# Kernel optimization log

Measured on AMD Instinct MI355X. Metric: run time of the kernel, lower is better.

## Reference

```python
import jax, jax.numpy as jnp
from jax import lax
import numpy as np

B, P, S, K = 16, 4096, 1024, 16   # clouds, points/cloud, fps samples/cloud (ratio 0.25), knn k
IN_F, OUT_F = 256, 512
EPS = 1e-5


def setup_inputs() -> dict:
    key = jax.random.key(0)
    k1, k2, k3 = jax.random.split(key, 3)
    features = jax.random.normal(k1, (B * P, IN_F), jnp.float32)
    positions = jax.random.normal(k2, (B * P, 3), jnp.float32)
    batch = jnp.repeat(jnp.arange(B, dtype=jnp.int32), P)
    W = jax.random.normal(k3, (IN_F, OUT_F), jnp.float32) / np.sqrt(IN_F)
    b = jnp.zeros((OUT_F,), jnp.float32)
    gamma = jnp.ones((OUT_F,), jnp.float32)
    beta = jnp.zeros((OUT_F,), jnp.float32)
    return {"features": features, "positions": positions, "batch": batch,
            "W": W, "b": b, "gamma": gamma, "beta": beta}


def _fps_local(pos):
    """Farthest point sampling on one cloud. pos: [P,3] -> [S] int32 local indices.
    Deterministic start at index 0 (torch_cluster fps with random_start disabled)."""
    def step(carry, _):
        min_d, last = carry
        d = jnp.sum((pos - pos[last]) ** 2, axis=-1)
        min_d = jnp.minimum(min_d, d)
        nxt = jnp.argmax(min_d).astype(jnp.int32)
        return (min_d, nxt), last
    init = (jnp.full((pos.shape[0],), jnp.inf, pos.dtype), jnp.int32(0))
    _, idx = lax.scan(step, init, None, length=S)
    return idx


def _knn_local(q, x):
    """K nearest neighbors of queries q [S,F] among x [P,F] (squared L2). -> [S,K] int32."""
    d = jnp.sum(q * q, -1, keepdims=True) - 2.0 * (q @ x.T) + jnp.sum(x * x, -1)
    _, idx = lax.top_k(-d, K)
    return idx


def reference(features, positions, batch, W, b, gamma, beta):
    pos_b = positions.reshape(B, P, 3)
    feat_b = features.reshape(B, P, IN_F)

    # --- FPS on positions, per cloud ---
    fps_loc = jax.vmap(_fps_local)(pos_b)                      # [B,S]
    offsets = (jnp.arange(B, dtype=jnp.int32) * P)[:, None]    # [B,1]
    fps_glob = (fps_loc + offsets).reshape(-1)                 # [B*S]

    # --- MLP: Linear -> BatchNorm1d (training batch stats, biased var) -> ReLU ---
    h = features @ W + b                                       # [N,OUT_F]
    mu = jnp.mean(h, axis=0)
    var = jnp.var(h, axis=0)
    h = jax.nn.relu(gamma * (h - mu) * lax.rsqrt(var + EPS) + beta)

    # --- brute-force KNN in feature space: queries = features[fps_indices] ---
    q = jnp.take_along_axis(feat_b, fps_loc[..., None], axis=1)   # [B,S,IN_F]
    nn_loc = jax.vmap(_knn_local)(q, feat_b)                      # [B,S,K]
    nn_glob = nn_loc + offsets[..., None]                         # [B,S,K]

    # --- scatter max-pool: each query has exactly K neighbors -> max over K ---
    nb = h[nn_glob.reshape(-1)].reshape(B, S, K, OUT_F)
    new_features = jnp.max(nb, axis=2).reshape(B * S, OUT_F)

    return new_features, positions[fps_glob], batch[fps_glob]
```

## Files before the change

kernel.cpp:

```cpp
#include <hip/hip_runtime.h>
#include <cstddef>


#define TD_B   16
#define TD_P   4096
#define TD_S   1024
#define TD_K   16
#define TD_INF 256
#define TD_OUTF 512

typedef __attribute__((ext_vector_type(8))) _Float16 half8;
typedef __attribute__((ext_vector_type(4))) float    f32x4;

__device__ __forceinline__ unsigned short f2bf(float x) {
    unsigned u = __float_as_uint(x);
    unsigned r = (u + 0x7fffu + ((u >> 16) & 1u)) >> 16;
    return (unsigned short)r;
}

struct FpsSm {
    float4 p4[TD_P];
    int    sel[TD_S];
    unsigned long long kw[2][8];
};
struct GemmSm {
    float As[16 * 260];
    float Bs[16 * 128];
};
union SmU {
    FpsSm f; GemmSm g;
    char pad_[84000];
};

#define TD_DPPSTEP(k, ctl, bc)                                                          \
    {                                                                                   \
        unsigned yh_ = (unsigned)__builtin_amdgcn_update_dpp(                           \
            0, (int)(unsigned)((k) >> 32), (ctl), 0xf, 0xf, (bc));                      \
        unsigned yl_ = (unsigned)__builtin_amdgcn_update_dpp(                           \
            0, (int)(unsigned)(k), (ctl), 0xf, 0xf, (bc));                              \
        unsigned long long y_ = ((unsigned long long)yh_ << 32) | yl_;                  \
        if (y_ > (k)) (k) = y_;                                                         \
    }

__global__ __launch_bounds__(512)
void td_fused(const float* __restrict__ feat, const float* __restrict__ pos,
              const float* __restrict__ W, const float* __restrict__ bias,
              unsigned short* __restrict__ H, float* __restrict__ XX,
              int* __restrict__ FPSI, float* __restrict__ outP,
              float* __restrict__ outB) {
    __shared__ SmU sm;
    const int bx = blockIdx.x;
    const int t  = threadIdx.x;

    if (bx < 16) {
        __builtin_amdgcn_s_setprio(2);
        const int b = bx;
        const int w = t >> 6;
        float px[8], py[8], pz[8], md[8];
        int ni[8];
#pragma unroll
        for (int j = 0; j < 8; ++j) {
            int p = j * 512 + t;
            const float* pp = pos + (size_t)(b * TD_P + p) * 3;
            float x = pp[0], y = pp[1], z = pp[2];
            px[j] = x; py[j] = y; pz[j] = z;
            sm.f.p4[p] = make_float4(x, y, z, 0.0f);
            md[j] = __builtin_inff();
            ni[j] = ~p;
        }
        if (t == 0) sm.f.sel[0] = 0;
        __syncthreads();
        float lx = sm.f.p4[0].x, ly = sm.f.p4[0].y, lz = sm.f.p4[0].z;
        for (int s = 0; s < TD_S - 1; ++s) {
            double k[8];
#pragma unroll
            for (int j = 0; j < 8; ++j) {
                float dx = __fsub_rn(px[j], lx);
                float dy = __fsub_rn(py[j], ly);
                float dz = __fsub_rn(pz[j], lz);
                float d  = __fadd_rn(__fadd_rn(__fmul_rn(dx, dx), __fmul_rn(dy, dy)),
                                     __fmul_rn(dz, dz));
                float m  = fminf(md[j], d);
                md[j] = m;
                k[j] = __hiloint2double(__float_as_int(m), ni[j]);
            }
            double k01 = fmax(k[0], k[1]), k23 = fmax(k[2], k[3]);
            double k45 = fmax(k[4], k[5]), k67 = fmax(k[6], k[7]);
            double kk  = fmax(fmax(k01, k23), fmax(k45, k67));
            unsigned long long tk = (unsigned long long)__double_as_longlong(kk);
            TD_DPPSTEP(tk, 0x111, true)
            TD_DPPSTEP(tk, 0x112, true)
            TD_DPPSTEP(tk, 0x114, true)
            TD_DPPSTEP(tk, 0x118, true)
            TD_DPPSTEP(tk, 0x142, false)
            TD_DPPSTEP(tk, 0x143, false)
            const int par = s & 1;
            if ((t & 63) == 63) sm.f.kw[par][w] = tk;
            __syncthreads();
            const unsigned long long* kwp = sm.f.kw[par];
            double g01 = fmax(__longlong_as_double((long long)kwp[0]),
                              __longlong_as_double((long long)kwp[1]));
            double g23 = fmax(__longlong_as_double((long long)kwp[2]),
                              __longlong_as_double((long long)kwp[3]));
            double g45 = fmax(__longlong_as_double((long long)kwp[4]),
                              __longlong_as_double((long long)kwp[5]));
            double g67 = fmax(__longlong_as_double((long long)kwp[6]),
                              __longlong_as_double((long long)kwp[7]));
            double gk  = fmax(fmax(g01, g23), fmax(g45, g67));
            unsigned idx = ~(unsigned)__double2loint(gk);
            if (t == 0) sm.f.sel[s + 1] = (int)idx;
            float4 wp = sm.f.p4[idx];
            lx = wp.x; ly = wp.y; lz = wp.z;
        }
        __syncthreads();
        for (int s = t; s < TD_S; s += 512) {
            int li = sm.f.sel[s];
            int og = b * TD_S + s;
            float4 wp = sm.f.p4[li];
            outP[og * 3 + 0] = wp.x;
            outP[og * 3 + 1] = wp.y;
            outP[og * 3 + 2] = wp.z;
            outB[og] = (float)b;
            FPSI[og] = b * TD_P + li;
        }
    } else if (bx < 16 + 1024) {
        const int gb = bx - 16;
        const int mb = gb >> 2, nb = gb & 3;
        const int tm = t >> 4, tn = t & 15;
        float acc[8][8];
#pragma unroll
        for (int i = 0; i < 8; ++i)
#pragma unroll
            for (int j = 0; j < 8; ++j) acc[i][j] = 0.0f;
        float* As = sm.g.As;
        float* Bs = sm.g.Bs;
        for (int kc = 0; kc < 16; ++kc) {
#pragma unroll
            for (int p2 = 0; p2 < 2; ++p2) {
                int f4 = t + 512 * p2;
                int r = f4 >> 2, c4 = f4 & 3;
                float4 v = *(const float4*)&feat[(size_t)(mb * 256 + r) * 256 + kc * 16 + c4 * 4];
                As[(c4 * 4 + 0) * 260 + r] = v.x;
                As[(c4 * 4 + 1) * 260 + r] = v.y;
                As[(c4 * 4 + 2) * 260 + r] = v.z;
                As[(c4 * 4 + 3) * 260 + r] = v.w;
            }
            {
                int kk = t >> 5, n4 = t & 31;
                float4 v = *(const float4*)&W[(size_t)(kc * 16 + kk) * 512 + nb * 128 + n4 * 4];
                *(float4*)&Bs[kk * 128 + n4 * 4] = v;
            }
            __syncthreads();
#pragma unroll
            for (int kk = 0; kk < 16; ++kk) {
                float4 a0 = *(float4*)&As[kk * 260 + tm * 8];
                float4 a1 = *(float4*)&As[kk * 260 + tm * 8 + 4];
                float4 b0 = *(float4*)&Bs[kk * 128 + tn * 8];
                float4 b1 = *(float4*)&Bs[kk * 128 + tn * 8 + 4];
                float av[8] = {a0.x, a0.y, a0.z, a0.w, a1.x, a1.y, a1.z, a1.w};
                float bv2[8] = {b0.x, b0.y, b0.z, b0.w, b1.x, b1.y, b1.z, b1.w};
#pragma unroll
                for (int i = 0; i < 8; ++i)
#pragma unroll
                    for (int j = 0; j < 8; ++j)
                        acc[i][j] = fmaf(av[i], bv2[j], acc[i][j]);
            }
            __syncthreads();
        }
        float4 bb0 = *(const float4*)&bias[nb * 128 + tn * 8];
        float4 bb1 = *(const float4*)&bias[nb * 128 + tn * 8 + 4];
        float bsv[8] = {bb0.x, bb0.y, bb0.z, bb0.w, bb1.x, bb1.y, bb1.z, bb1.w};
#pragma unroll
        for (int i = 0; i < 8; ++i) {
            int row = mb * 256 + tm * 8 + i;
            uint4 pk;
            pk.x = (unsigned)f2bf(acc[i][0] + bsv[0]) | ((unsigned)f2bf(acc[i][1] + bsv[1]) << 16);
            pk.y = (unsigned)f2bf(acc[i][2] + bsv[2]) | ((unsigned)f2bf(acc[i][3] + bsv[3]) << 16);
            pk.z = (unsigned)f2bf(acc[i][4] + bsv[4]) | ((unsigned)f2bf(acc[i][5] + bsv[5]) << 16);
            pk.w = (unsigned)f2bf(acc[i][6] + bsv[6]) | ((unsigned)f2bf(acc[i][7] + bsv[7]) << 16);
            *(uint4*)&H[(size_t)row * 512 + nb * 128 + tn * 8] = pk;
        }
    } else {
        const int xb = bx - 1040;
        const int w = t >> 6, lane = t & 63;
#pragma unroll
        for (int it = 0; it < 8; ++it) {
            int r = xb * 64 + w * 8 + it;
            float4 v = *(const float4*)&feat[(size_t)r * 256 + lane * 4];
            float s = v.x * v.x + v.y * v.y + v.z * v.z + v.w * v.w;
#pragma unroll
            for (int off = 32; off > 0; off >>= 1) s += __shfl_down(s, off, 64);
            if (lane == 0) XX[r] = s;
        }
    }
}

__global__ __launch_bounds__(256)
void td_stats(const unsigned short* __restrict__ H, float* __restrict__ P1,
              float* __restrict__ P2) {
    const int rb = blockIdx.x, t = threadIdx.x;
    float s1a = 0, s2a = 0, s1b = 0, s2b = 0;
    for (int r = 0; r < 256; ++r) {
        const unsigned* hp = (const unsigned*)(H + (size_t)(rb * 256 + r) * 512);
        unsigned u = hp[t];
        float lo = __uint_as_float(u << 16);
        float hi = __uint_as_float(u & 0xffff0000u);
        s1a += lo; s2a = fmaf(lo, lo, s2a);
        s1b += hi; s2b = fmaf(hi, hi, s2b);
    }
    P1[rb * 512 + 2 * t] = s1a; P1[rb * 512 + 2 * t + 1] = s1b;
    P2[rb * 512 + 2 * t] = s2a; P2[rb * 512 + 2 * t + 1] = s2b;
}

__global__ __launch_bounds__(512)
void td_bnfin(const float* __restrict__ P1, const float* __restrict__ P2,
              const float* __restrict__ gamma, const float* __restrict__ beta,
              float* __restrict__ SS) {
    const int ch = threadIdx.x;
    float s1 = 0, s2 = 0;
    for (int rb = 0; rb < 256; ++rb) { s1 += P1[rb * 512 + ch]; s2 += P2[rb * 512 + ch]; }
    const float invN = 1.0f / 65536.0f;
    float mu  = s1 * invN;
    float var = s2 * invN - mu * mu;
    float sc  = gamma[ch] * (1.0f / sqrtf(var + 1e-5f));
    float sh  = beta[ch] - mu * sc;
    SS[ch] = sc; SS[512 + ch] = sh;
}

__global__ __launch_bounds__(256, 2)
void td_knn2(const float* __restrict__ feat, const float* __restrict__ XX,
             const int* __restrict__ FPSI, float* __restrict__ PD,
             int* __restrict__ PI) {
    __shared__ union {
        _Float16 x[2][32][264];
        float    dt[128][33];
    } sm;
    __shared__ float QQs[128];
    __shared__ int   QR[128];

    const int bx = blockIdx.x, t = threadIdx.x;
    const int b = bx & 15, r2 = bx >> 4;
    const int qq8 = r2 >> 2, seg = r2 & 3;
    const int cb = b * TD_P;
    const int segbase = cb + seg * 1024;

    if (t < 128) {
        int gr = FPSI[b * TD_S + qq8 * 128 + t];
        QR[t] = gr; QQs[t] = XX[gr];
    }
    __syncthreads();

    const int w = t >> 6, lane = t & 63;
    const int m = lane & 15, quad = lane >> 4;

    half8 qh[2][8], ql[2][8];
#pragma unroll
    for (int qs = 0; qs < 2; ++qs) {
        const float* qp = feat + (size_t)QR[w * 32 + qs * 16 + m] * 256;
#pragma unroll
        for (int ks = 0; ks < 8; ++ks) {
            float4 f0 = *(const float4*)(qp + ks * 32 + quad * 8);
            float4 f1 = *(const float4*)(qp + ks * 32 + quad * 8 + 4);
            float fv[8] = {f0.x, f0.y, f0.z, f0.w, f1.x, f1.y, f1.z, f1.w};
            half8 h, l;
#pragma unroll
            for (int j = 0; j < 8; ++j) {
                _Float16 hv = (_Float16)fv[j];
                h[j] = hv;
                l[j] = (_Float16)(fv[j] - (float)hv);
            }
            qh[qs][ks] = h; ql[qs][ks] = l;
        }
    }

    float sd[16]; int si[16];
#pragma unroll
    for (int r = 0; r < 16; ++r) { sd[r] = __builtin_inff(); si[r] = 0x7fffffff; }

    const int xrow = t >> 3, part = t & 7;

    for (int ct = 0; ct < 32; ++ct) {
        __syncthreads();
        {
            const float* xp = feat + (size_t)(segbase + ct * 32 + xrow) * 256 + part * 32;
#pragma unroll
            for (int s2 = 0; s2 < 4; ++s2) {
                float4 f0 = *(const float4*)(xp + s2 * 8);
                float4 f1 = *(const float4*)(xp + s2 * 8 + 4);
                float fv[8] = {f0.x, f0.y, f0.z, f0.w, f1.x, f1.y, f1.z, f1.w};
                half8 h, l;
#pragma unroll
                for (int j = 0; j < 8; ++j) {
                    _Float16 hv = (_Float16)fv[j];
                    h[j] = hv;
                    l[j] = (_Float16)(fv[j] - (float)hv);
                }
                *(half8*)&sm.x[0][xrow][part * 32 + s2 * 8] = h;
                *(half8*)&sm.x[1][xrow][part * 32 + s2 * 8] = l;
            }
        }
        __syncthreads();
        f32x4 acc[2][2];
#pragma unroll
        for (int qs = 0; qs < 2; ++qs) { acc[qs][0] = (f32x4)0.0f; acc[qs][1] = (f32x4)0.0f; }
#pragma unroll
        for (int ks = 0; ks < 8; ++ks) {
            half8 xh0 = *(half8*)&sm.x[0][m][ks * 32 + quad * 8];
            half8 xl0 = *(half8*)&sm.x[1][m][ks * 32 + quad * 8];
            half8 xh1 = *(half8*)&sm.x[0][16 + m][ks * 32 + quad * 8];
            half8 xl1 = *(half8*)&sm.x[1][16 + m][ks * 32 + quad * 8];
#pragma unroll
            for (int qs = 0; qs < 2; ++qs) {
                acc[qs][0] = __builtin_amdgcn_mfma_f32_16x16x32_f16(ql[qs][ks], xh0, acc[qs][0], 0, 0, 0);
                acc[qs][0] = __builtin_amdgcn_mfma_f32_16x16x32_f16(qh[qs][ks], xl0, acc[qs][0], 0, 0, 0);
                acc[qs][0] = __builtin_amdgcn_mfma_f32_16x16x32_f16(qh[qs][ks], xh0, acc[qs][0], 0, 0, 0);
                acc[qs][1] = __builtin_amdgcn_mfma_f32_16x16x32_f16(ql[qs][ks], xh1, acc[qs][1], 0, 0, 0);
                acc[qs][1] = __builtin_amdgcn_mfma_f32_16x16x32_f16(qh[qs][ks], xl1, acc[qs][1], 0, 0, 0);
                acc[qs][1] = __builtin_amdgcn_mfma_f32_16x16x32_f16(qh[qs][ks], xh1, acc[qs][1], 0, 0, 0);
            }
        }
        __syncthreads();
        {
            float xx0 = XX[segbase + ct * 32 + m];
            float xx1 = XX[segbase + ct * 32 + 16 + m];
#pragma unroll
            for (int qs = 0; qs < 2; ++qs) {
                int qb = w * 32 + qs * 16 + quad * 4;
#pragma unroll
                for (int reg = 0; reg < 4; ++reg) {
                    float qq = QQs[qb + reg];
                    sm.dt[qb + reg][m]      = (qq - 2.0f * acc[qs][0][reg]) + xx0;
                    sm.dt[qb + reg][16 + m] = (qq - 2.0f * acc[qs][1][reg]) + xx1;
                }
            }
        }
        __syncthreads();
        if (t < 128) {
            const int ibase = segbase + ct * 32;
            for (int j = 0; j < 32; ++j) {
                float d = sm.dt[t][j];
                if (d < sd[15]) {
                    sd[15] = d; si[15] = ibase + j;
#pragma unroll
                    for (int r = 15; r > 0; --r) {
                        if (sd[r] < sd[r - 1]) {
                            float td2 = sd[r]; sd[r] = sd[r - 1]; sd[r - 1] = td2;
                            int ti = si[r]; si[r] = si[r - 1]; si[r - 1] = ti;
                        }
                    }
                }
            }
        }
    }
    if (t < 128) {
        size_t o = ((size_t)(b * TD_S + qq8 * 128 + t)) * 64 + seg * 16;
#pragma unroll
        for (int r = 0; r < 16; ++r) { PD[o + r] = sd[r]; PI[o + r] = si[r]; }
    }
}

__global__ __launch_bounds__(64)
void td_merge(const float* __restrict__ PD, const int* __restrict__ PI,
              int* __restrict__ NN) {
    __shared__ float ld_[64][65];
    __shared__ int   li_[64][65];
    const int bx = blockIdx.x, t = threadIdx.x;
    for (int j = 0; j < 64; ++j) {
        ld_[j][t] = PD[(size_t)bx * 4096 + j * 64 + t];
        li_[j][t] = PI[(size_t)bx * 4096 + j * 64 + t];
    }
    __syncthreads();
    int p[4] = {0, 0, 0, 0};
    int og = (bx * 64 + t) * TD_K;
    for (int r = 0; r < 16; ++r) {
        float bd = __builtin_inff(); int bi = 0x7fffffff; int bs = 0;
#pragma unroll
        for (int s = 0; s < 4; ++s) {
            if (p[s] < 16) {
                float d = ld_[t][s * 16 + p[s]];
                int   i = li_[t][s * 16 + p[s]];
                if (d < bd || (d == bd && i < bi)) { bd = d; bi = i; bs = s; }
            }
        }
        p[bs]++;
        NN[og + r] = bi;
    }
}

__global__ __launch_bounds__(256)
void td_maxpool(const unsigned short* __restrict__ H, const int* __restrict__ NN,
                const float* __restrict__ SS, float* __restrict__ outF) {
    __shared__ int nbr[16];
    const int bx = blockIdx.x, t = threadIdx.x;
    const int g = (bx & 15) * 1024 + (bx >> 4);
    if (t < 16) nbr[t] = NN[g * 16 + t];
    __syncthreads();
    float sc0 = SS[2 * t], sc1 = SS[2 * t + 1];
    float sh0 = SS[512 + 2 * t], sh1 = SS[512 + 2 * t + 1];
    float m0 = 0.0f, m1 = 0.0f;
#pragma unroll
    for (int k = 0; k < 16; ++k) {
        int row = nbr[k];
        unsigned u = ((const unsigned*)(H + (size_t)row * 512))[t];
        float lo = __uint_as_float(u << 16);
        float hi = __uint_as_float(u & 0xffff0000u);
        m0 = fmaxf(m0, fmaf(sc0, lo, sh0));
        m1 = fmaxf(m1, fmaf(sc1, hi, sh1));
    }
    float2 o; o.x = m0; o.y = m1;
    *(float2*)&outF[(size_t)g * 512 + 2 * t] = o;
}

extern "C" void kernel_launch(void* const* d_in, const int* in_sizes, int n_in,
                              void* d_out, int out_size, void* d_ws, size_t ws_size,
                              hipStream_t stream) {
    const float* feat  = (const float*)d_in[0];
    const float* pos   = (const float*)d_in[1];
    const float* W     = (const float*)d_in[3];
    const float* bias  = (const float*)d_in[4];
    const float* gamma = (const float*)d_in[5];
    const float* beta  = (const float*)d_in[6];

    char* ws = (char*)d_ws;
    unsigned short* H = (unsigned short*)ws;
    float* XX  = (float*)(ws + 67108864);
    int*   FPSI= (int*)  (ws + 67371008);
    int*   NN  = (int*)  (ws + 67436544);
    float* P1  = (float*)(ws + 68485120);
    float* P2  = (float*)(ws + 69533696);
    float* SS  = (float*)(ws + 70582272);
    float* PD  = (float*)(ws + 70586368);
    int*   PI  = (int*)  (ws + 74780672);

    float* outF = (float*)d_out;
    float* outP = outF + (size_t)TD_B * TD_S * TD_OUTF;
    float* outB = outP + (size_t)TD_B * TD_S * 3;

    td_fused  <<<2064, 512, 0, stream>>>(feat, pos, W, bias, H, XX, FPSI, outP, outB);
    td_stats  <<<256, 256, 0, stream>>>(H, P1, P2);
    td_bnfin  <<<1, 512, 0, stream>>>(P1, P2, gamma, beta, SS);
    td_knn2   <<<512, 256, 0, stream>>>(feat, XX, FPSI, PD, PI);
    td_merge  <<<256, 64, 0, stream>>>(PD, PI, NN);
    td_maxpool<<<TD_B * TD_S, 256, 0, stream>>>(H, NN, SS, outF);
}
```

Baseline: 1.117 ms.

## Pack FPS into 4 waves with float2 math, reorder MFMAs, batch maxpool queries

The FPS block now uses only 256 of its 512 threads. Each active thread handles 16 points as packed float2 vectors, so the sequential critical loop reduces across 4 waves instead of 8 and can use packed FP32 ops. Separately, the KNN MFMA chain is interleaved across the four independent accumulators to hide MFMA dependency latency. The maxpool kernel now processes 4 queries per block, which cuts block count and per-block overhead. The trade-off is that each FPS thread does more serial work, and the half-idle block could still hold a CU slot.

```diff
diff --git a/kernel.cpp b/kernel.cpp
--- a/kernel.cpp
+++ b/kernel.cpp
@@ -11,6 +11,7 @@
 
 typedef __attribute__((ext_vector_type(8))) _Float16 half8;
 typedef __attribute__((ext_vector_type(4))) float    f32x4;
+typedef __attribute__((ext_vector_type(2))) float    v2f;
 
 __device__ __forceinline__ unsigned short f2bf(float x) {
     unsigned u = __float_as_uint(x);
@@ -56,61 +57,74 @@
         __builtin_amdgcn_s_setprio(2);
         const int b = bx;
         const int w = t >> 6;
-        float px[8], py[8], pz[8], md[8];
-        int ni[8];
-#pragma unroll
-        for (int j = 0; j < 8; ++j) {
-            int p = j * 512 + t;
-            const float* pp = pos + (size_t)(b * TD_P + p) * 3;
-            float x = pp[0], y = pp[1], z = pp[2];
-            px[j] = x; py[j] = y; pz[j] = z;
-            sm.f.p4[p] = make_float4(x, y, z, 0.0f);
-            md[j] = __builtin_inff();
-            ni[j] = ~p;
-        }
-        if (t == 0) sm.f.sel[0] = 0;
-        __syncthreads();
-        float lx = sm.f.p4[0].x, ly = sm.f.p4[0].y, lz = sm.f.p4[0].z;
+        v2f px[8], py[8], pz[8], md[8];
+        int ni0[8], ni1[8];
+        float lx = 0.0f, ly = 0.0f, lz = 0.0f;
+        if (t < 256) {
+#pragma unroll
+            for (int j = 0; j < 8; ++j) {
+                int p0 = j * 512 + t, p1 = p0 + 256;
+                const float* q0 = pos + (size_t)(b * TD_P + p0) * 3;
+                const float* q1 = pos + (size_t)(b * TD_P + p1) * 3;
+                float x0 = q0[0], y0 = q0[1], z0 = q0[2];
+                float x1 = q1[0], y1 = q1[1], z1 = q1[2];
+                px[j] = (v2f){x0, x1}; py[j] = (v2f){y0, y1}; pz[j] = (v2f){z0, z1};
+                sm.f.p4[p0] = make_float4(x0, y0, z0, 0.0f);
+                sm.f.p4[p1] = make_float4(x1, y1, z1, 0.0f);
+                md[j] = (v2f){__builtin_inff(), __builtin_inff()};
+                ni0[j] = ~p0; ni1[j] = ~p1;
+            }
+            if (t == 0) sm.f.sel[0] = 0;
+        }
+        __syncthreads();
+        if (t < 256) { float4 wp = sm.f.p4[0]; lx = wp.x; ly = wp.y; lz = wp.z; }
         for (int s = 0; s < TD_S - 1; ++s) {
-            double k[8];
-#pragma unroll
-            for (int j = 0; j < 8; ++j) {
-                float dx = __fsub_rn(px[j], lx);
-                float dy = __fsub_rn(py[j], ly);
-                float dz = __fsub_rn(pz[j], lz);
-                float d  = __fadd_rn(__fadd_rn(__fmul_rn(dx, dx), __fmul_rn(dy, dy)),
-                                     __fmul_rn(dz, dz));
-                float m  = fminf(md[j], d);
-                md[j] = m;
-                k[j] = __hiloint2double(__float_as_int(m), ni[j]);
-            }
-            double k01 = fmax(k[0], k[1]), k23 = fmax(k[2], k[3]);
-            double k45 = fmax(k[4], k[5]), k67 = fmax(k[6], k[7]);
-            double kk  = fmax(fmax(k01, k23), fmax(k45, k67));
-            unsigned long long tk = (unsigned long long)__double_as_longlong(kk);
-            TD_DPPSTEP(tk, 0x111, true)
-            TD_DPPSTEP(tk, 0x112, true)
-            TD_DPPSTEP(tk, 0x114, true)
-            TD_DPPSTEP(tk, 0x118, true)
-            TD_DPPSTEP(tk, 0x142, false)
-            TD_DPPSTEP(tk, 0x143, false)
             const int par = s & 1;
-            if ((t & 63) == 63) sm.f.kw[par][w] = tk;
+            if (t < 256) {
+                double k[16];
+                {
+#pragma clang fp contract(off)
+                    v2f l2x = (v2f){lx, lx}, l2y = (v2f){ly, ly}, l2z = (v2f){lz, lz};
+#pragma unroll
+                    for (int j = 0; j < 8; ++j) {
+                        v2f dx = px[j] - l2x;
+                        v2f dy = py[j] - l2y;
+                        v2f dz = pz[j] - l2z;
+                        v2f sx = dx * dx;
+                        v2f sy = dy * dy;
+                        v2f sz = dz * dz;
+                        v2f dd = (sx + sy) + sz;
+                        md[j] = __builtin_elementwise_min(md[j], dd);
+                        k[2 * j]     = __hiloint2double(__float_as_int(md[j].x), ni0[j]);
+                        k[2 * j + 1] = __hiloint2double(__float_as_int(md[j].y), ni1[j]);
+                    }
+                }
+#pragma unroll
+                for (int st = 8; st > 0; st >>= 1)
+#pragma unroll
+                    for (int i = 0; i < st; ++i) k[i] = fmax(k[i], k[i + st]);
+                unsigned long long tk = (unsigned long long)__double_as_longlong(k[0]);
+                TD_DPPSTEP(tk, 0x111, true)
+                TD_DPPSTEP(tk, 0x112, true)
+                TD_DPPSTEP(tk, 0x114, true)
+                TD_DPPSTEP(tk, 0x118, true)
+                TD_DPPSTEP(tk, 0x142, false)
+                TD_DPPSTEP(tk, 0x143, false)
+                if ((t & 63) == 63) sm.f.kw[par][w] = tk;
+            }
             __syncthreads();
-            const unsigned long long* kwp = sm.f.kw[par];
-            double g01 = fmax(__longlong_as_double((long long)kwp[0]),
-                              __longlong_as_double((long long)kwp[1]));
-            double g23 = fmax(__longlong_as_double((long long)kwp[2]),
-                              __longlong_as_double((long long)kwp[3]));
-            double g45 = fmax(__longlong_as_double((long long)kwp[4]),
-                              __longlong_as_double((long long)kwp[5]));
-            double g67 = fmax(__longlong_as_double((long long)kwp[6]),
-                              __longlong_as_double((long long)kwp[7]));
-            double gk  = fmax(fmax(g01, g23), fmax(g45, g67));
-            unsigned idx = ~(unsigned)__double2loint(gk);
-            if (t == 0) sm.f.sel[s + 1] = (int)idx;
-            float4 wp = sm.f.p4[idx];
-            lx = wp.x; ly = wp.y; lz = wp.z;
+            if (t < 256) {
+                const unsigned long long* kwp = sm.f.kw[par];
+                double g01 = fmax(__longlong_as_double((long long)kwp[0]),
+                                  __longlong_as_double((long long)kwp[1]));
+                double g23 = fmax(__longlong_as_double((long long)kwp[2]),
+                                  __longlong_as_double((long long)kwp[3]));
+                double gk  = fmax(g01, g23);
+                unsigned idx = ~(unsigned)__double2loint(gk);
+                if (t == 0) sm.f.sel[s + 1] = (int)idx;
+                float4 wp = sm.f.p4[idx];
+                lx = wp.x; ly = wp.y; lz = wp.z;
+            }
         }
         __syncthreads();
         for (int s = t; s < TD_S; s += 512) {
@@ -301,23 +315,26 @@
         }
         __syncthreads();
         f32x4 acc[2][2];
-#pragma unroll
-        for (int qs = 0; qs < 2; ++qs) { acc[qs][0] = (f32x4)0.0f; acc[qs][1] = (f32x4)0.0f; }
+        acc[0][0] = (f32x4)0.0f; acc[0][1] = (f32x4)0.0f;
+        acc[1][0] = (f32x4)0.0f; acc[1][1] = (f32x4)0.0f;
 #pragma unroll
         for (int ks = 0; ks < 8; ++ks) {
             half8 xh0 = *(half8*)&sm.x[0][m][ks * 32 + quad * 8];
             half8 xl0 = *(half8*)&sm.x[1][m][ks * 32 + quad * 8];
             half8 xh1 = *(half8*)&sm.x[0][16 + m][ks * 32 + quad * 8];
             half8 xl1 = *(half8*)&sm.x[1][16 + m][ks * 32 + quad * 8];
-#pragma unroll
-            for (int qs = 0; qs < 2; ++qs) {
-                acc[qs][0] = __builtin_amdgcn_mfma_f32_16x16x32_f16(ql[qs][ks], xh0, acc[qs][0], 0, 0, 0);
-                acc[qs][0] = __builtin_amdgcn_mfma_f32_16x16x32_f16(qh[qs][ks], xl0, acc[qs][0], 0, 0, 0);
-                acc[qs][0] = __builtin_amdgcn_mfma_f32_16x16x32_f16(qh[qs][ks], xh0, acc[qs][0], 0, 0, 0);
-                acc[qs][1] = __builtin_amdgcn_mfma_f32_16x16x32_f16(ql[qs][ks], xh1, acc[qs][1], 0, 0, 0);
-                acc[qs][1] = __builtin_amdgcn_mfma_f32_16x16x32_f16(qh[qs][ks], xl1, acc[qs][1], 0, 0, 0);
-                acc[qs][1] = __builtin_amdgcn_mfma_f32_16x16x32_f16(qh[qs][ks], xh1, acc[qs][1], 0, 0, 0);
-            }
+            acc[0][0] = __builtin_amdgcn_mfma_f32_16x16x32_f16(ql[0][ks], xh0, acc[0][0], 0, 0, 0);
+            acc[0][1] = __builtin_amdgcn_mfma_f32_16x16x32_f16(ql[0][ks], xh1, acc[0][1], 0, 0, 0);
+            acc[1][0] = __builtin_amdgcn_mfma_f32_16x16x32_f16(ql[1][ks], xh0, acc[1][0], 0, 0, 0);
+            acc[1][1] = __builtin_amdgcn_mfma_f32_16x16x32_f16(ql[1][ks], xh1, acc[1][1], 0, 0, 0);
+            acc[0][0] = __builtin_amdgcn_mfma_f32_16x16x32_f16(qh[0][ks], xl0, acc[0][0], 0, 0, 0);
+            acc[0][1] = __builtin_amdgcn_mfma_f32_16x16x32_f16(qh[0][ks], xl1, acc[0][1], 0, 0, 0);
+            acc[1][0] = __builtin_amdgcn_mfma_f32_16x16x32_f16(qh[1][ks], xl0, acc[1][0], 0, 0, 0);
+            acc[1][1] = __builtin_amdgcn_mfma_f32_16x16x32_f16(qh[1][ks], xl1, acc[1][1], 0, 0, 0);
+            acc[0][0] = __builtin_amdgcn_mfma_f32_16x16x32_f16(qh[0][ks], xh0, acc[0][0], 0, 0, 0);
+            acc[0][1] = __builtin_amdgcn_mfma_f32_16x16x32_f16(qh[0][ks], xh1, acc[0][1], 0, 0, 0);
+            acc[1][0] = __builtin_amdgcn_mfma_f32_16x16x32_f16(qh[1][ks], xh0, acc[1][0], 0, 0, 0);
+            acc[1][1] = __builtin_amdgcn_mfma_f32_16x16x32_f16(qh[1][ks], xh1, acc[1][1], 0, 0, 0);
         }
         __syncthreads();
         {
@@ -390,25 +407,29 @@
 __global__ __launch_bounds__(256)
 void td_maxpool(const unsigned short* __restrict__ H, const int* __restrict__ NN,
                 const float* __restrict__ SS, float* __restrict__ outF) {
-    __shared__ int nbr[16];
+    __shared__ int nbr[64];
     const int bx = blockIdx.x, t = threadIdx.x;
-    const int g = (bx & 15) * 1024 + (bx >> 4);
-    if (t < 16) nbr[t] = NN[g * 16 + t];
+    const int cloud = bx & 15, blk = bx >> 4;
+    const int qbase = cloud * 1024 + blk * 4;
+    if (t < 64) nbr[t] = NN[(size_t)qbase * 16 + t];
     __syncthreads();
     float sc0 = SS[2 * t], sc1 = SS[2 * t + 1];
     float sh0 = SS[512 + 2 * t], sh1 = SS[512 + 2 * t + 1];
-    float m0 = 0.0f, m1 = 0.0f;
-#pragma unroll
-    for (int k = 0; k < 16; ++k) {
-        int row = nbr[k];
-        unsigned u = ((const unsigned*)(H + (size_t)row * 512))[t];
-        float lo = __uint_as_float(u << 16);
-        float hi = __uint_as_float(u & 0xffff0000u);
-        m0 = fmaxf(m0, fmaf(sc0, lo, sh0));
-        m1 = fmaxf(m1, fmaf(sc1, hi, sh1));
-    }
-    float2 o; o.x = m0; o.y = m1;
-    *(float2*)&outF[(size_t)g * 512 + 2 * t] = o;
+#pragma unroll
+    for (int qi = 0; qi < 4; ++qi) {
+        float m0 = 0.0f, m1 = 0.0f;
+#pragma unroll
+        for (int k = 0; k < 16; ++k) {
+            int row = nbr[qi * 16 + k];
+            unsigned u = ((const unsigned*)(H + (size_t)row * 512))[t];
+            float lo = __uint_as_float(u << 16);
+            float hi = __uint_as_float(u & 0xffff0000u);
+            m0 = fmaxf(m0, fmaf(sc0, lo, sh0));
+            m1 = fmaxf(m1, fmaf(sc1, hi, sh1));
+        }
+        float2 o; o.x = m0; o.y = m1;
+        *(float2*)&outF[(size_t)(qbase + qi) * 512 + 2 * t] = o;
+    }
 }
 
 extern "C" void kernel_launch(void* const* d_in, const int* in_sizes, int n_in,
@@ -441,5 +462,5 @@
     td_bnfin  <<<1, 512, 0, stream>>>(P1, P2, gamma, beta, SS);
     td_knn2   <<<512, 256, 0, stream>>>(feat, XX, FPSI, PD, PI);
     td_merge  <<<256, 64, 0, stream>>>(PD, PI, NN);
-    td_maxpool<<<TD_B * TD_S, 256, 0, stream>>>(H, NN, SS, outF);
-}
+    td_maxpool<<<TD_B * 256, 256, 0, stream>>>(H, NN, SS, outF);
+}
```

Result: no change. 1.107 ms (-0.9%).
